# Performance work log

Hardware: AMD Instinct MI355X
Metric: run time of the kernel (lower is better)

The kernel has to match this reference:

```python
import jax, jax.numpy as jnp
import numpy as np

N = 100000      # nodes
E = 1600000     # edges (avg degree 16)
DIN = 32
DOUT = 32


def setup_inputs() -> dict:
    key = jax.random.key(0)
    k1, k2, k3 = jax.random.split(key, 3)
    x = jax.random.normal(k1, (N, DIN), dtype=jnp.float32)
    edge_index = jax.random.randint(k2, (2, E), 0, N)  # [2, E] (src, dst)
    W = jax.random.normal(k3, (DIN, DOUT), dtype=jnp.float32) / np.sqrt(DIN).astype(np.float32)
    b = jnp.zeros((DOUT,), dtype=jnp.float32)
    return {"x": x, "edge_index": edge_index, "W": W, "b": b}


def reference(x, edge_index, W, b):
    # GCNConv with norm='both' (DGL GraphConv semantics):
    # out = D_dst^{-1/2} * A * (D_src^{-1/2} * X * W) + b
    src, dst = edge_index[0], edge_index[1]
    ones = jnp.ones((edge_index.shape[1],), dtype=x.dtype)
    out_deg = jax.ops.segment_sum(ones, src, num_segments=N)  # out-degree of src nodes
    in_deg = jax.ops.segment_sum(ones, dst, num_segments=N)   # in-degree of dst nodes
    norm_src = jnp.where(out_deg > 0, out_deg ** -0.5, 0.0)   # [N]
    norm_dst = jnp.where(in_deg > 0, in_deg ** -0.5, 0.0)     # [N]
    # feature transform before aggregation (in_feats >= out_feats path)
    h = (x * norm_src[:, None]) @ W                           # [N, DOUT]
    # sparse neighbor aggregation: gather along src, scatter-add to dst
    agg = jax.ops.segment_sum(h[src], dst, num_segments=N)    # [N, DOUT]
    return agg * norm_dst[:, None] + b
```

## Files before the change

kernel.cpp:

```cpp
#include <hip/hip_runtime.h>
#include <hip/hip_bf16.h>

#define DIN 32
#define DOUT 32
#define BINSHIFT 8
#define BINW 256
#define NBMAX 512
#define PTHREADS 512
#define PK 8
#define PB (PTHREADS * PK)
#define SRCBITS 17
#define SRCMASK ((1u << SRCBITS) - 1u)
#define CAP_LDS 8192
#define AK (CAP_LDS / 1024)

__device__ __forceinline__ float bf_lo(unsigned v) { return __uint_as_float(v << 16); }
__device__ __forceinline__ float bf_hi(unsigned v) { return __uint_as_float(v & 0xffff0000u); }
__device__ __forceinline__ unsigned f2bf_rne(float f) {
    unsigned u = __float_as_uint(f);
    return (u + 0x7fffu + ((u >> 16) & 1u)) >> 16;
}
__device__ __forceinline__ int wave_incl_scan(int v) {
#pragma unroll
    for (int o = 1; o < 64; o <<= 1) {
        int u = __shfl_up(v, o, 64);
        if ((threadIdx.x & 63) >= o) v += u;
    }
    return v;
}

__global__ void init_caps_kernel(int* __restrict__ baseS, int* __restrict__ baseD,
                                 int* __restrict__ curS, int* __restrict__ curD,
                                 int NB, int cap) {
    int i = threadIdx.x;
    if (i <= NB) {
        int v = i * cap;
        baseS[i] = v; baseD[i] = v;
        if (i < NB) { curS[i] = v; curD[i] = v; }
    }
}

__global__ void hist_coarse_kernel(const int* __restrict__ src, const int* __restrict__ dst,
                                   int E, int* __restrict__ gcntS, int* __restrict__ gcntD) {
    __shared__ int hS[NBMAX], hD[NBMAX];
    for (int i = threadIdx.x; i < NBMAX; i += 256) { hS[i] = 0; hD[i] = 0; }
    __syncthreads();
    int stride = gridDim.x * blockDim.x;
    for (int e = blockIdx.x * blockDim.x + threadIdx.x; e < E; e += stride) {
        atomicAdd(&hS[src[e] >> BINSHIFT], 1);
        atomicAdd(&hD[dst[e] >> BINSHIFT], 1);
    }
    __syncthreads();
    for (int i = threadIdx.x; i < NBMAX; i += 256) {
        if (hS[i]) atomicAdd(&gcntS[i], hS[i]);
        if (hD[i]) atomicAdd(&gcntD[i], hD[i]);
    }
}

__global__ void scan_coarse_kernel(const int* __restrict__ gcntS, const int* __restrict__ gcntD,
                                   int* __restrict__ baseS, int* __restrict__ baseD,
                                   int* __restrict__ curS, int* __restrict__ curD,
                                   int NB, int E) {
    __shared__ int wsS[8], wsD[8];
    int t = threadIdx.x;
    int a = (t < NB) ? gcntS[t] : 0;
    int c = (t < NB) ? gcntD[t] : 0;
    int sS = wave_incl_scan(a);
    int sD = wave_incl_scan(c);
    int w = t >> 6;
    if ((t & 63) == 63) { wsS[w] = sS; wsD[w] = sD; }
    __syncthreads();
    int addS = 0, addD = 0;
#pragma unroll
    for (int i = 0; i < 8; ++i) if (i < w) { addS += wsS[i]; addD += wsD[i]; }
    if (t < NB) {
        baseS[t] = sS - a + addS; curS[t] = sS - a + addS;
        baseD[t] = sD - c + addD; curD[t] = sD - c + addD;
    }
    if (t == 0) { baseS[NB] = E; baseD[NB] = E; }
}

__global__ void partition_both_kernel(const int* __restrict__ src, const int* __restrict__ dst,
                                      int E, int* __restrict__ curS, int* __restrict__ curD,
                                      unsigned char* __restrict__ binnedS,
                                      int* __restrict__ binnedD) {
    __shared__ int cntS[NBMAX], cntD[NBMAX];
    __shared__ int gbS[NBMAX], gbD[NBMAX];
    __shared__ int wsS[8], wsD[8];
    __shared__ int stage[PB];
    __shared__ unsigned short sbin[PB];
    int t = threadIdx.x;
    cntS[t] = 0; cntD[t] = 0;
    __syncthreads();

    int base_e = blockIdx.x * PB;
    int nvalid = E - base_e; if (nvalid > PB) nvalid = PB;

    int vs[PK], vd[PK], rkS[PK], rkD[PK];
#pragma unroll
    for (int i = 0; i < PK; ++i) {
        int e = base_e + i * PTHREADS + t;
        if (e < E) {
            int s = src[e], d = dst[e];
            vs[i] = s; vd[i] = d;
            rkS[i] = atomicAdd(&cntS[s >> BINSHIFT], 1);
            rkD[i] = atomicAdd(&cntD[d >> BINSHIFT], 1);
        } else vs[i] = -1;
    }
    __syncthreads();

    int cS = cntS[t], cD = cntD[t];
    int sS = wave_incl_scan(cS);
    int sD = wave_incl_scan(cD);
    int w = t >> 6;
    if ((t & 63) == 63) { wsS[w] = sS; wsD[w] = sD; }
    __syncthreads();
    int addS = 0, addD = 0;
#pragma unroll
    for (int i = 0; i < 8; ++i) if (i < w) { addS += wsS[i]; addD += wsD[i]; }
    int lS = sS - cS + addS, lD = sD - cD + addD;
    int gS = cS ? atomicAdd(&curS[t], cS) : 0;
    int gD = cD ? atomicAdd(&curD[t], cD) : 0;
    gbS[t] = gS - lS; gbD[t] = gD - lD;
    cntS[t] = lS; cntD[t] = lD;
    __syncthreads();

#pragma unroll
    for (int i = 0; i < PK; ++i) {
        if (vs[i] >= 0) {
            int b = vs[i] >> BINSHIFT;
            int slot = cntS[b] + rkS[i];
            stage[slot] = vs[i] & (BINW - 1);
            sbin[slot] = (unsigned short)b;
        }
    }
    __syncthreads();
    for (int i = t; i < nvalid; i += PTHREADS)
        binnedS[gbS[sbin[i]] + i] = (unsigned char)stage[i];
    __syncthreads();

#pragma unroll
    for (int i = 0; i < PK; ++i) {
        if (vs[i] >= 0) {
            int b = vd[i] >> BINSHIFT;
            int slot = cntD[b] + rkD[i];
            stage[slot] = ((vd[i] & (BINW - 1)) << SRCBITS) | vs[i];
            sbin[slot] = (unsigned short)b;
        }
    }
    __syncthreads();
    for (int i = t; i < nvalid; i += PTHREADS)
        binnedD[gbD[sbin[i]] + i] = stage[i];
}

__global__ void cnt_transform_kernel(const unsigned char* __restrict__ binnedS,
                                     const int* __restrict__ baseS, const int* __restrict__ endS,
                                     const float* __restrict__ x, const float* __restrict__ W,
                                     unsigned* __restrict__ h, int n) {
    __shared__ float xs[BINW][33];
    __shared__ float Ws[32][33];
    __shared__ int   cnt[BINW];
    int t = threadIdx.x;
    int b = blockIdx.x;
    int beg = baseS[b], end = endS[b];
    int lo = b << BINSHIFT;

    if (t < BINW) cnt[t] = 0;
    for (int i = t; i < 32 * 32; i += 512) Ws[i >> 5][i & 31] = W[i];
    __syncthreads();

    for (int e = beg + t; e < end; e += 512) atomicAdd(&cnt[binnedS[e]], 1);

    int rcnt = n - lo; if (rcnt > BINW) rcnt = BINW; if (rcnt < 0) rcnt = 0;
    const float4* x4 = reinterpret_cast<const float4*>(x);
    for (int i = t; i < rcnt * 8; i += 512) {
        float4 v = x4[(size_t)lo * 8 + i];
        int r = i >> 3, c = (i & 7) << 2;
        xs[r][c] = v.x; xs[r][c + 1] = v.y; xs[r][c + 2] = v.z; xs[r][c + 3] = v.w;
    }
    __syncthreads();

    int r = t >> 1, half = t & 1;
    if (r < rcnt) {
        float acc[16];
#pragma unroll
        for (int j = 0; j < 16; ++j) acc[j] = 0.f;
#pragma unroll
        for (int k = 0; k < 32; ++k) {
            float xv = xs[r][k];
            const float* wr = &Ws[k][half * 16];
#pragma unroll
            for (int j = 0; j < 16; ++j) acc[j] += xv * wr[j];
        }
        int d = cnt[r];
        float nrm = (d > 0) ? rsqrtf((float)d) : 0.f;
        unsigned o[8];
#pragma unroll
        for (int j = 0; j < 8; ++j)
            o[j] = f2bf_rne(acc[2 * j] * nrm) | (f2bf_rne(acc[2 * j + 1] * nrm) << 16);
        uint4* h4 = reinterpret_cast<uint4*>(h);
        h4[(size_t)(lo + r) * 4 + half * 2]     = uint4{o[0], o[1], o[2], o[3]};
        h4[(size_t)(lo + r) * 4 + half * 2 + 1] = uint4{o[4], o[5], o[6], o[7]};
    }
}

__global__ void csr_agg_kernel(const int* __restrict__ binnedD, const int* __restrict__ baseD,
                               const int* __restrict__ endD, const uint4* __restrict__ hb4,
                               const float* __restrict__ bias, float* __restrict__ out, int n) {
    __shared__ int cnt[BINW];
    __shared__ int start[BINW];
    __shared__ int wsum[4];
    __shared__ int lesrc[CAP_LDS];

    int t = threadIdx.x;
    int b = blockIdx.x;
    int beg = baseD[b], end = endD[b];
    int lo = b << BINSHIFT;
    int q  = t & 3;
    int ng = t >> 2;

    float4 A0 = {0,0,0,0}, A1 = {0,0,0,0};
    float4 B0 = {0,0,0,0}, B1 = {0,0,0,0};
    int deg = 0;

    for (int cb = beg; cb < end; cb += CAP_LDS) {
        int ce = cb + CAP_LDS; if (ce > end) ce = end;
        if (t < BINW) cnt[t] = 0;
        __syncthreads();
        unsigned pv[AK]; int rk[AK];
#pragma unroll
        for (int i = 0; i < AK; ++i) {
            int e = cb + i * 1024 + t;
            if (e < ce) {
                pv[i] = (unsigned)binnedD[e];
                rk[i] = atomicAdd(&cnt[pv[i] >> SRCBITS], 1);
            } else pv[i] = 0xFFFFFFFFu;
        }
        __syncthreads();
        int v = 0, s = 0;
        if (t < BINW) {
            v = cnt[t];
            s = wave_incl_scan(v);
            if ((t & 63) == 63) wsum[t >> 6] = s;
        }
        __syncthreads();
        if (t < BINW) {
            int w = t >> 6, add = 0;
            if (w > 0) add += wsum[0];
            if (w > 1) add += wsum[1];
            if (w > 2) add += wsum[2];
            start[t] = s - v + add;
        }
        __syncthreads();
#pragma unroll
        for (int i = 0; i < AK; ++i)
            if (pv[i] != 0xFFFFFFFFu)
                lesrc[start[pv[i] >> SRCBITS] + rk[i]] = (int)(pv[i] & SRCMASK);
        __syncthreads();

        int kb = start[ng], kc = cnt[ng];
        deg += kc;
        int k = kb, ke = kb + kc;
        for (; k + 4 <= ke; k += 4) {
            int s0 = lesrc[k], s1 = lesrc[k + 1], s2 = lesrc[k + 2], s3 = lesrc[k + 3];
            uint4 v0 = hb4[(size_t)s0 * 4 + q];
            uint4 v1 = hb4[(size_t)s1 * 4 + q];
            uint4 v2 = hb4[(size_t)s2 * 4 + q];
            uint4 v3 = hb4[(size_t)s3 * 4 + q];
            A0.x += bf_lo(v0.x); A0.y += bf_hi(v0.x); A0.z += bf_lo(v0.y); A0.w += bf_hi(v0.y);
            A1.x += bf_lo(v0.z); A1.y += bf_hi(v0.z); A1.z += bf_lo(v0.w); A1.w += bf_hi(v0.w);
            B0.x += bf_lo(v1.x); B0.y += bf_hi(v1.x); B0.z += bf_lo(v1.y); B0.w += bf_hi(v1.y);
            B1.x += bf_lo(v1.z); B1.y += bf_hi(v1.z); B1.z += bf_lo(v1.w); B1.w += bf_hi(v1.w);
            A0.x += bf_lo(v2.x); A0.y += bf_hi(v2.x); A0.z += bf_lo(v2.y); A0.w += bf_hi(v2.y);
            A1.x += bf_lo(v2.z); A1.y += bf_hi(v2.z); A1.z += bf_lo(v2.w); A1.w += bf_hi(v2.w);
            B0.x += bf_lo(v3.x); B0.y += bf_hi(v3.x); B0.z += bf_lo(v3.y); B0.w += bf_hi(v3.y);
            B1.x += bf_lo(v3.z); B1.y += bf_hi(v3.z); B1.z += bf_lo(v3.w); B1.w += bf_hi(v3.w);
        }
        for (; k < ke; ++k) {
            uint4 v4 = hb4[(size_t)lesrc[k] * 4 + q];
            A0.x += bf_lo(v4.x); A0.y += bf_hi(v4.x); A0.z += bf_lo(v4.y); A0.w += bf_hi(v4.y);
            A1.x += bf_lo(v4.z); A1.y += bf_hi(v4.z); A1.z += bf_lo(v4.w); A1.w += bf_hi(v4.w);
        }
        __syncthreads();
    }

    A0.x += B0.x; A0.y += B0.y; A0.z += B0.z; A0.w += B0.w;
    A1.x += B1.x; A1.y += B1.y; A1.z += B1.z; A1.w += B1.w;

    int node = lo + ng;
    if (node < n) {
        float nrm = (deg > 0) ? rsqrtf((float)deg) : 0.f;
        const float4* b4 = reinterpret_cast<const float4*>(bias);
        float4 bv0 = b4[2 * q], bv1 = b4[2 * q + 1];
        float4 o0, o1;
        o0.x = A0.x * nrm + bv0.x; o0.y = A0.y * nrm + bv0.y;
        o0.z = A0.z * nrm + bv0.z; o0.w = A0.w * nrm + bv0.w;
        o1.x = A1.x * nrm + bv1.x; o1.y = A1.y * nrm + bv1.y;
        o1.z = A1.z * nrm + bv1.z; o1.w = A1.w * nrm + bv1.w;
        float4* o4 = reinterpret_cast<float4*>(out);
        o4[(size_t)node * 8 + 2 * q]     = o0;
        o4[(size_t)node * 8 + 2 * q + 1] = o1;
    }
}

__global__ void deg_kernel(const int* __restrict__ src, const int* __restrict__ dst,
                           int* __restrict__ degs, int* __restrict__ degd, int E) {
    int i = blockIdx.x * blockDim.x + threadIdx.x;
    if (i < E) {
        atomicAdd(&degs[src[i]], 1);
        atomicAdd(&degd[dst[i]], 1);
    }
}

__global__ void transform_f32_kernel(const float* __restrict__ x, const float* __restrict__ W,
                                     const int* __restrict__ degs, float* __restrict__ h, int n) {
    __shared__ float Ws[32][33];
    __shared__ float xs[8][32];
    int col = threadIdx.x & 31;
    int r   = threadIdx.x >> 5;
    for (int i = threadIdx.x; i < 32 * 32; i += 256) Ws[i >> 5][i & 31] = W[i];
    int row = blockIdx.x * 8 + r;
    xs[r][col] = (row < n) ? x[row * 32 + col] : 0.f;
    __syncthreads();
    if (row < n) {
        float acc = 0.f;
#pragma unroll
        for (int k = 0; k < 32; ++k) acc += xs[r][k] * Ws[k][col];
        int d = degs[row];
        float nrm = (d > 0) ? rsqrtf((float)d) : 0.f;
        h[row * 32 + col] = acc * nrm;
    }
}

__global__ void scatter_kernel(const int* __restrict__ src, const int* __restrict__ dst,
                               const float* __restrict__ h, float* __restrict__ out, int E) {
    int t = blockIdx.x * blockDim.x + threadIdx.x;
    int e = t >> 3;
    int q = t & 7;
    if (e < E) {
        int s = src[e];
        int d = dst[e];
        const float4 v = *reinterpret_cast<const float4*>(&h[s * 32 + q * 4]);
        float* o = &out[d * 32 + q * 4];
        atomicAdd(o + 0, v.x);
        atomicAdd(o + 1, v.y);
        atomicAdd(o + 2, v.z);
        atomicAdd(o + 3, v.w);
    }
}

__global__ void finalize_kernel(float* __restrict__ out, const int* __restrict__ degd,
                                const float* __restrict__ b, int n) {
    int t = blockIdx.x * blockDim.x + threadIdx.x;
    if (t < n * 32) {
        int row = t >> 5;
        int col = t & 31;
        int d = degd[row];
        float nrm = (d > 0) ? rsqrtf((float)d) : 0.f;
        out[t] = out[t] * nrm + b[col];
    }
}

extern "C" void kernel_launch(void* const* d_in, const int* in_sizes, int n_in,
                              void* d_out, int out_size, void* d_ws, size_t ws_size,
                              hipStream_t stream) {
    const float* x  = (const float*)d_in[0];
    const int*   ei = (const int*)d_in[1];
    const float* W  = (const float*)d_in[2];
    const float* bb = (const float*)d_in[3];
    float* out = (float*)d_out;

    const int n = in_sizes[0] / DIN;
    const int E = in_sizes[1] / 2;
    const int* src = ei;
    const int* dst = ei + E;

    const int NB = (n + BINW - 1) >> BINSHIFT;

    int cap = (int)((((long long)E / NB) * 3 / 2 + 255) & ~255LL);
    if (cap < 1024) cap = 1024;

    size_t szH = ((size_t)n * DOUT * sizeof(__hip_bfloat16) + 15) & ~(size_t)15;

    auto layout = [&](size_t nBin, char* p0, unsigned char** binnedS, int** binnedD,
                      unsigned** h, int** gcntS, int** gcntD, int** baseS, int** baseD,
                      int** curS, int** curD) -> size_t {
        char* p = p0;
        *binnedS = (unsigned char*)p;  p += (nBin + PB + 15) & ~(size_t)15;
        *binnedD = (int*)p;            p += (nBin * 4 + PB * 4 + 15) & ~(size_t)15;
        *h       = (unsigned*)p;       p += szH;
        *gcntS   = (int*)p;            p += NBMAX * sizeof(int);
        *gcntD   = (int*)p;            p += NBMAX * sizeof(int);
        *baseS   = (int*)p;            p += (NBMAX + 1) * sizeof(int);
        *baseD   = (int*)p;            p += (NBMAX + 1) * sizeof(int);
        *curS    = (int*)p;            p += NBMAX * sizeof(int);
        *curD    = (int*)p;            p += NBMAX * sizeof(int);
        return (size_t)(p - p0);
    };

    unsigned char* binnedS;
    int *binnedD, *gcntS, *gcntD, *baseS, *baseD, *curS, *curD;
    unsigned* h;

    const int partBlocks = (E + PB - 1) / PB;
    bool ok = (NB <= NBMAX) && (n <= (1 << SRCBITS));

    if (ok) {
        size_t need = layout((size_t)NB * cap, (char*)d_ws, &binnedS, &binnedD, &h,
                             &gcntS, &gcntD, &baseS, &baseD, &curS, &curD);
        if (need <= ws_size) {
            init_caps_kernel<<<1, NBMAX, 0, stream>>>(baseS, baseD, curS, curD, NB, cap);
            partition_both_kernel<<<partBlocks, PTHREADS, 0, stream>>>(src, dst, E, curS, curD,
                                                                       binnedS, binnedD);
            cnt_transform_kernel<<<NB, 512, 0, stream>>>(binnedS, baseS, curS, x, W, h, n);
            csr_agg_kernel<<<NB, 1024, 0, stream>>>(binnedD, baseD, curD, (const uint4*)h,
                                                    bb, out, n);
            return;
        }
        need = layout((size_t)E, (char*)d_ws, &binnedS, &binnedD, &h,
                      &gcntS, &gcntD, &baseS, &baseD, &curS, &curD);
        if (need <= ws_size) {
            hipMemsetAsync(gcntS, 0, 2 * NBMAX * sizeof(int), stream);
            hist_coarse_kernel<<<512, 256, 0, stream>>>(src, dst, E, gcntS, gcntD);
            scan_coarse_kernel<<<1, NBMAX, 0, stream>>>(gcntS, gcntD, baseS, baseD,
                                                        curS, curD, NB, E);
            partition_both_kernel<<<partBlocks, PTHREADS, 0, stream>>>(src, dst, E, curS, curD,
                                                                       binnedS, binnedD);
            cnt_transform_kernel<<<NB, 512, 0, stream>>>(binnedS, baseS, curS, x, W, h, n);
            csr_agg_kernel<<<NB, 1024, 0, stream>>>(binnedD, baseD, curD, (const uint4*)h,
                                                    bb, out, n);
            return;
        }
    }

    {
        float* hf   = (float*)d_ws;
        int*   dgs  = (int*)(hf + (size_t)n * DOUT);
        int*   degd = dgs + n;
        hipMemsetAsync(dgs, 0, (size_t)2 * n * sizeof(int), stream);
        hipMemsetAsync(d_out, 0, (size_t)out_size * sizeof(float), stream);
        deg_kernel<<<(E + 255) / 256, 256, 0, stream>>>(src, dst, dgs, degd, E);
        transform_f32_kernel<<<(n + 7) / 8, 256, 0, stream>>>(x, W, dgs, hf, n);
        long long st = (long long)E * 8;
        scatter_kernel<<<(int)((st + 255) / 256), 256, 0, stream>>>(src, dst, hf, out, E);
        finalize_kernel<<<(n * 32 + 255) / 256, 256, 0, stream>>>(out, degd, bb, n);
    }
}
```

Before: 75.14 us.

## Split bf16 feature table into two column halves and gather per half

The transformed feature table h is stored as two separate column-half tables of 32 bytes per node instead of one 64-byte row. The aggregation kernel makes two passes, one per half-table, with pairs of threads splitting each node's edge list and merging partial sums by warp shuffle. The aim is a smaller working set per pass so the gathered half-table stays in cache better. The cost is twice the passes over the LDS edge list, extra shuffles, and half the lanes idle at the store.

Result: slower. 82.15 us (+9.3%).

```diff
diff --git a/kernel.cpp b/kernel.cpp
--- a/kernel.cpp
+++ b/kernel.cpp
@@ -28,6 +28,10 @@
     }
     return v;
 }
+__device__ __forceinline__ void acc8(float4& lo4, float4& hi4, uint4 v) {
+    lo4.x += bf_lo(v.x); lo4.y += bf_hi(v.x); lo4.z += bf_lo(v.y); lo4.w += bf_hi(v.y);
+    hi4.x += bf_lo(v.z); hi4.y += bf_hi(v.z); hi4.z += bf_lo(v.w); hi4.w += bf_hi(v.w);
+}
 
 __global__ void init_caps_kernel(int* __restrict__ baseS, int* __restrict__ baseD,
                                  int* __restrict__ curS, int* __restrict__ curD,
@@ -199,8 +203,9 @@
         for (int j = 0; j < 8; ++j)
             o[j] = f2bf_rne(acc[2 * j] * nrm) | (f2bf_rne(acc[2 * j + 1] * nrm) << 16);
         uint4* h4 = reinterpret_cast<uint4*>(h);
-        h4[(size_t)(lo + r) * 4 + half * 2]     = uint4{o[0], o[1], o[2], o[3]};
-        h4[(size_t)(lo + r) * 4 + half * 2 + 1] = uint4{o[4], o[5], o[6], o[7]};
+        size_t base = (size_t)half * n * 2 + (size_t)(lo + r) * 2;
+        h4[base]     = uint4{o[0], o[1], o[2], o[3]};
+        h4[base + 1] = uint4{o[4], o[5], o[6], o[7]};
     }
 }
 
@@ -218,10 +223,14 @@
     int lo = b << BINSHIFT;
     int q  = t & 3;
     int ng = t >> 2;
+    int qp = q & 1;
+    int sub = q >> 1;
 
     float4 A0 = {0,0,0,0}, A1 = {0,0,0,0};
     float4 B0 = {0,0,0,0}, B1 = {0,0,0,0};
     int deg = 0;
+
+    const uint4* tab1 = hb4 + (size_t)n * 2;
 
     for (int cb = beg; cb < end; cb += CAP_LDS) {
         int ce = cb + CAP_LDS; if (ce > end) ce = end;
@@ -260,46 +269,81 @@
 
         int kb = start[ng], kc = cnt[ng];
         deg += kc;
-        int k = kb, ke = kb + kc;
-        for (; k + 4 <= ke; k += 4) {
-            int s0 = lesrc[k], s1 = lesrc[k + 1], s2 = lesrc[k + 2], s3 = lesrc[k + 3];
-            uint4 v0 = hb4[(size_t)s0 * 4 + q];
-            uint4 v1 = hb4[(size_t)s1 * 4 + q];
-            uint4 v2 = hb4[(size_t)s2 * 4 + q];
-            uint4 v3 = hb4[(size_t)s3 * 4 + q];
-            A0.x += bf_lo(v0.x); A0.y += bf_hi(v0.x); A0.z += bf_lo(v0.y); A0.w += bf_hi(v0.y);
-            A1.x += bf_lo(v0.z); A1.y += bf_hi(v0.z); A1.z += bf_lo(v0.w); A1.w += bf_hi(v0.w);
-            B0.x += bf_lo(v1.x); B0.y += bf_hi(v1.x); B0.z += bf_lo(v1.y); B0.w += bf_hi(v1.y);
-            B1.x += bf_lo(v1.z); B1.y += bf_hi(v1.z); B1.z += bf_lo(v1.w); B1.w += bf_hi(v1.w);
-            A0.x += bf_lo(v2.x); A0.y += bf_hi(v2.x); A0.z += bf_lo(v2.y); A0.w += bf_hi(v2.y);
-            A1.x += bf_lo(v2.z); A1.y += bf_hi(v2.z); A1.z += bf_lo(v2.w); A1.w += bf_hi(v2.w);
-            B0.x += bf_lo(v3.x); B0.y += bf_hi(v3.x); B0.z += bf_lo(v3.y); B0.w += bf_hi(v3.y);
-            B1.x += bf_lo(v3.z); B1.y += bf_hi(v3.z); B1.z += bf_lo(v3.w); B1.w += bf_hi(v3.w);
-        }
-        for (; k < ke; ++k) {
-            uint4 v4 = hb4[(size_t)lesrc[k] * 4 + q];
-            A0.x += bf_lo(v4.x); A0.y += bf_hi(v4.x); A0.z += bf_lo(v4.y); A0.w += bf_hi(v4.y);
-            A1.x += bf_lo(v4.z); A1.y += bf_hi(v4.z); A1.z += bf_lo(v4.w); A1.w += bf_hi(v4.w);
-        }
-        __syncthreads();
-    }
-
-    A0.x += B0.x; A0.y += B0.y; A0.z += B0.z; A0.w += B0.w;
-    A1.x += B1.x; A1.y += B1.y; A1.z += B1.z; A1.w += B1.w;
+        int ke = kb + kc;
+
+        {
+            float4 C0 = {0,0,0,0}, C1 = {0,0,0,0};
+            int k = kb + sub;
+            for (; k + 6 < ke; k += 8) {
+                int s0 = lesrc[k],     s1 = lesrc[k + 2];
+                int s2 = lesrc[k + 4], s3 = lesrc[k + 6];
+                uint4 v0 = hb4[(size_t)s0 * 2 + qp];
+                uint4 v1 = hb4[(size_t)s1 * 2 + qp];
+                uint4 v2 = hb4[(size_t)s2 * 2 + qp];
+                uint4 v3 = hb4[(size_t)s3 * 2 + qp];
+                acc8(A0, A1, v0); acc8(C0, C1, v1);
+                acc8(A0, A1, v2); acc8(C0, C1, v3);
+            }
+            for (; k < ke; k += 2) {
+                uint4 vv = hb4[(size_t)lesrc[k] * 2 + qp];
+                acc8(A0, A1, vv);
+            }
+            A0.x += C0.x; A0.y += C0.y; A0.z += C0.z; A0.w += C0.w;
+            A1.x += C1.x; A1.y += C1.y; A1.z += C1.z; A1.w += C1.w;
+        }
+        {
+            float4 C0 = {0,0,0,0}, C1 = {0,0,0,0};
+            int k = kb + sub;
+            for (; k + 6 < ke; k += 8) {
+                int s0 = lesrc[k],     s1 = lesrc[k + 2];
+                int s2 = lesrc[k + 4], s3 = lesrc[k + 6];
+                uint4 v0 = tab1[(size_t)s0 * 2 + qp];
+                uint4 v1 = tab1[(size_t)s1 * 2 + qp];
+                uint4 v2 = tab1[(size_t)s2 * 2 + qp];
+                uint4 v3 = tab1[(size_t)s3 * 2 + qp];
+                acc8(B0, B1, v0); acc8(C0, C1, v1);
+                acc8(B0, B1, v2); acc8(C0, C1, v3);
+            }
+            for (; k < ke; k += 2) {
+                uint4 vv = tab1[(size_t)lesrc[k] * 2 + qp];
+                acc8(B0, B1, vv);
+            }
+            B0.x += C0.x; B0.y += C0.y; B0.z += C0.z; B0.w += C0.w;
+            B1.x += C1.x; B1.y += C1.y; B1.z += C1.z; B1.w += C1.w;
+        }
+        __syncthreads();
+    }
+
+    A0.x += __shfl_xor(A0.x, 2); A0.y += __shfl_xor(A0.y, 2);
+    A0.z += __shfl_xor(A0.z, 2); A0.w += __shfl_xor(A0.w, 2);
+    A1.x += __shfl_xor(A1.x, 2); A1.y += __shfl_xor(A1.y, 2);
+    A1.z += __shfl_xor(A1.z, 2); A1.w += __shfl_xor(A1.w, 2);
+    B0.x += __shfl_xor(B0.x, 2); B0.y += __shfl_xor(B0.y, 2);
+    B0.z += __shfl_xor(B0.z, 2); B0.w += __shfl_xor(B0.w, 2);
+    B1.x += __shfl_xor(B1.x, 2); B1.y += __shfl_xor(B1.y, 2);
+    B1.z += __shfl_xor(B1.z, 2); B1.w += __shfl_xor(B1.w, 2);
 
     int node = lo + ng;
-    if (node < n) {
+    if (node < n && sub == 0) {
         float nrm = (deg > 0) ? rsqrtf((float)deg) : 0.f;
         const float4* b4 = reinterpret_cast<const float4*>(bias);
-        float4 bv0 = b4[2 * q], bv1 = b4[2 * q + 1];
-        float4 o0, o1;
+        float4 bv0 = b4[qp * 2], bv1 = b4[qp * 2 + 1];
+        float4 bv2 = b4[4 + qp * 2], bv3 = b4[4 + qp * 2 + 1];
+        float4 o0, o1, o2, o3;
         o0.x = A0.x * nrm + bv0.x; o0.y = A0.y * nrm + bv0.y;
         o0.z = A0.z * nrm + bv0.z; o0.w = A0.w * nrm + bv0.w;
         o1.x = A1.x * nrm + bv1.x; o1.y = A1.y * nrm + bv1.y;
         o1.z = A1.z * nrm + bv1.z; o1.w = A1.w * nrm + bv1.w;
+        o2.x = B0.x * nrm + bv2.x; o2.y = B0.y * nrm + bv2.y;
+        o2.z = B0.z * nrm + bv2.z; o2.w = B0.w * nrm + bv2.w;
+        o3.x = B1.x * nrm + bv3.x; o3.y = B1.y * nrm + bv3.y;
+        o3.z = B1.z * nrm + bv3.z; o3.w = B1.w * nrm + bv3.w;
         float4* o4 = reinterpret_cast<float4*>(out);
-        o4[(size_t)node * 8 + 2 * q]     = o0;
-        o4[(size_t)node * 8 + 2 * q + 1] = o1;
+        size_t rb = (size_t)node * 8;
+        o4[rb + qp * 2]     = o0;
+        o4[rb + qp * 2 + 1] = o1;
+        o4[rb + 4 + qp * 2]     = o2;
+        o4[rb + 4 + qp * 2 + 1] = o3;
     }
 }
 
```
